# Kernel tuning notes

Measured on AMD Instinct MI355X. Metric: run time of the kernel, lower is better.

The kernel has to match this reference:

```python
import jax, jax.numpy as jnp
import numpy as np

N_PTS = 131072      # query points
N_DIMS = 3          # spatial dims
N_FEATS = 1000      # total_n_features = prod(feature_grid_shape '10,10,10')
FDIM = 64           # n_features per grid point
PE_TERMS = 6        # num_positional_encoding_terms
HID = 128           # nodes_per_layer
OUT = 1             # n_outputs
D_IN = PE_TERMS * N_DIMS * 2 + FDIM  # 100


def _linear_init(k, d_in, d_out):
    # xavier-ish init for a [out, in] torch-style weight
    return jax.random.normal(k, (d_out, d_in), dtype=jnp.float32) * np.float32(1.0 / np.sqrt(d_in))


def setup_inputs() -> dict:
    key = jax.random.key(0)
    ks = jax.random.split(key, 10)
    x = jax.random.uniform(ks[0], (N_PTS, N_DIMS), minval=-1.0, maxval=1.0, dtype=jnp.float32)
    feature_locations = jax.random.uniform(ks[1], (N_FEATS, N_DIMS), minval=-1.0, maxval=1.0, dtype=jnp.float32)
    feature_vectors = jax.random.normal(ks[2], (N_FEATS, FDIM), dtype=jnp.float32)
    W0 = _linear_init(ks[3], D_IN, HID); b0 = jnp.zeros((HID,), jnp.float32)
    W1 = _linear_init(ks[4], HID, HID);  b1 = jnp.zeros((HID,), jnp.float32)
    W2 = _linear_init(ks[5], HID, HID);  b2 = jnp.zeros((HID,), jnp.float32)
    W3 = _linear_init(ks[6], HID, HID);  b3 = jnp.zeros((HID,), jnp.float32)
    W4 = _linear_init(ks[7], HID, OUT);  b4 = jnp.zeros((OUT,), jnp.float32)
    return dict(x=x, feature_locations=feature_locations, feature_vectors=feature_vectors,
                W0=W0, b0=b0, W1=W1, b1=b1, W2=W2, b2=b2, W3=W3, b3=b3, W4=W4, b4=b4)


def _snake_alt(h):
    # SnakeAlt activation: 0.5*x + sin(x)^2
    return 0.5 * h + jnp.sin(h) ** 2


def _positional_encoding(x):
    # NeRF-style PE: sin/cos of (2^l * pi * x), l = 0..PE_TERMS-1 -> [N, PE_TERMS*N_DIMS*2]
    freqs = (2.0 ** jnp.arange(PE_TERMS, dtype=jnp.float32)) * jnp.pi
    ang = x[:, :, None] * freqs  # [N, n_dims, L]
    return jnp.concatenate([jnp.sin(ang), jnp.cos(ang)], axis=-1).reshape(x.shape[0], -1)


def reference(x, feature_locations, feature_vectors, W0, b0, W1, b1, W2, b2, W3, b3, W4, b4):
    # L2 distance from each point to each feature location, via expanded quadratic form
    # (same math as sqrt(sum((x-loc)^2)) without materializing [N, F, n_dims])
    d2 = (jnp.sum(x * x, axis=-1, keepdims=True)
          - 2.0 * (x @ feature_locations.T)
          + jnp.sum(feature_locations * feature_locations, axis=-1))
    d2 = jnp.maximum(d2, 0.0)
    inv_d = 1.0 / (jnp.sqrt(d2) + 1e-6)
    w = jax.nn.softmax(inv_d, axis=1)            # [N, F]
    feats = w @ feature_vectors                  # [N, FDIM]
    pe = _positional_encoding(x)                 # [N, 36]
    y = jnp.concatenate([pe, feats], axis=1)     # [N, 100]
    y = _snake_alt(y @ W0.T + b0)
    y = _snake_alt(y @ W1.T + b1)
    y = _snake_alt(y @ W2.T + b2)
    y = _snake_alt(y @ W3.T + b3)
    return y @ W4.T + b4                         # [N, 1]
```

## Files before the change

### kernel.cpp

```cpp
#include <hip/hip_runtime.h>
#include <hip/hip_bf16.h>

#define N_PTS   131072
#define N_FEATS 1000
#define FDIM    64
#define HID     128
#define NCHUNK  32
#define PI_F    3.14159265358979f
#define L2E     1.44269504f

typedef short  short8  __attribute__((ext_vector_type(8)));
typedef float  floatx4 __attribute__((ext_vector_type(4)));

__device__ __forceinline__ unsigned int packbf2(float a, float b) {
    float2 t; t.x = a; t.y = b;
    __hip_bfloat162 h = __float22bfloat162_rn(t);
    union { __hip_bfloat162 hh; unsigned int u; } cv; cv.hh = h;
    return cv.u;
}
__device__ __forceinline__ unsigned short f2bf(float f) {
    return (unsigned short)packbf2(f, f);
}
__device__ __forceinline__ float bf2f(unsigned short h) {
    return __uint_as_float(((unsigned int)h) << 16);
}
__device__ __forceinline__ floatx4 min3_4(floatx4 a, floatx4 b, floatx4 c) {
    floatx4 r;
    r[0] = fminf(fminf(a[0], b[0]), c[0]);
    r[1] = fminf(fminf(a[1], b[1]), c[1]);
    r[2] = fminf(fminf(a[2], b[2]), c[2]);
    r[3] = fminf(fminf(a[3], b[3]), c[3]);
    return r;
}


__device__ __forceinline__ short8 xfrag_build(int quad, float x0, float x1, float x2) {
    unsigned short h0, m0, l0, h1, m1, l1, h2, m2, l2, Ah, Am, Al;
    { h0 = f2bf(x0); float r = x0 - bf2f(h0); m0 = f2bf(r); l0 = f2bf(r - bf2f(m0)); }
    { h1 = f2bf(x1); float r = x1 - bf2f(h1); m1 = f2bf(r); l1 = f2bf(r - bf2f(m1)); }
    { h2 = f2bf(x2); float r = x2 - bf2f(h2); m2 = f2bf(r); l2 = f2bf(r - bf2f(m2)); }
    float A = x0*x0 + x1*x1 + x2*x2;
    { Ah = f2bf(A); float r = A - bf2f(Ah); Am = f2bf(r); Al = f2bf(r - bf2f(Am)); }
    union { short8 v; unsigned short u[8]; } f;
    if (quad == 0) {
        f.u[0]=h0; f.u[1]=m0; f.u[2]=h0; f.u[3]=l0; f.u[4]=m0; f.u[5]=h0; f.u[6]=h1; f.u[7]=m1;
    } else if (quad == 1) {
        f.u[0]=h1; f.u[1]=l1; f.u[2]=m1; f.u[3]=h1; f.u[4]=h2; f.u[5]=m2; f.u[6]=h2; f.u[7]=l2;
    } else if (quad == 2) {
        f.u[0]=m2; f.u[1]=h2; f.u[2]=0x3F80; f.u[3]=0x3F80; f.u[4]=0x3F80; f.u[5]=Ah; f.u[6]=Am; f.u[7]=Al;
    } else {
        f.v = (short8)0;
    }
    return f.v;
}

__global__ void prep_all(const float* __restrict__ locs, const float* __restrict__ fv,
                         const float* __restrict__ W0, const float* __restrict__ W1,
                         const float* __restrict__ W2, const float* __restrict__ W3,
                         unsigned short* __restrict__ DB,
                         unsigned short* __restrict__ fvB, unsigned short* __restrict__ WB)
{
    int i = blockIdx.x * 256 + threadIdx.x;
    if (i < 65536) {
        int j = i & 7, n = (i >> 3) & 63, cq = i >> 9;
        int c = cq >> 2, quad = cq & 3;
        int fl = (j < 4) ? quad*4 + j : 16 + quad*4 + (j - 4);
        int f = c*32 + fl;
        float v = (f < N_FEATS) ? fv[f*FDIM + n] : 0.f;
        fvB[i] = f2bf(v);
    } else if (i < 131072) {
        int r = i - 65536;
        int j = r & 7, lane = (r >> 3) & 63, c = (r >> 9) & 3;
        int nt = (r >> 11) & 1, q = (r >> 12) & 3, L = r >> 14;
        int n = (q*2 + nt)*16 + (lane & 15);
        int k = c*32 + (lane >> 4)*8 + j;
        const float* W = (L == 0) ? W0 : (L == 1) ? W1 : (L == 2) ? W2 : W3;
        int Kin = (L == 0) ? 100 : 128;
        float v = (k < Kin) ? W[n*Kin + k] : 0.f;
        WB[r] = f2bf(v);
    } else if (i < 163840) {
        int r = i - 131072;
        int j = r & 7, ft = (r >> 3) & 15, quad = (r >> 7) & 3, fg = r >> 9;
        int f = fg*16 + ft, s = quad*8 + j;
        float lx, ly, lz;
        if (f < N_FEATS) { lx = locs[f*3+0]; ly = locs[f*3+1]; lz = locs[f*3+2]; }
        else             { lx = 1e9f; ly = 1e9f; lz = 1e9f; }
        unsigned short val = 0;
        if (s < 18) {
            int d = s / 6, t = s - d*6;
            float l2 = -2.f * ((d == 0) ? lx : (d == 1) ? ly : lz);
            unsigned short h = f2bf(l2);
            float r1 = l2 - bf2f(h);
            unsigned short m = f2bf(r1);
            unsigned short l = f2bf(r1 - bf2f(m));
            val = (t == 2 || t == 4) ? m : (t == 5) ? l : h;
        } else if (s < 21) {
            float SL = lx*lx + ly*ly + lz*lz;
            unsigned short h = f2bf(SL);
            float r1 = SL - bf2f(h);
            unsigned short m = f2bf(r1);
            unsigned short l = f2bf(r1 - bf2f(m));
            val = (s == 18) ? h : (s == 19) ? m : l;
        } else if (s < 24) {
            val = 0x3F80;
        }
        DB[r] = val;
    }
}

__global__ __launch_bounds__(256, 3)
void afvsrn_mfma(const float* __restrict__ x,
                 const unsigned short* __restrict__ DB,
                 const unsigned short* __restrict__ fvB,
                 const unsigned short* __restrict__ WB,
                 const float* __restrict__ b0, const float* __restrict__ b1,
                 const float* __restrict__ b2, const float* __restrict__ b3,
                 const float* __restrict__ W4, const float* __restrict__ b4,
                 float* __restrict__ out)
{
    __shared__ unsigned short act[128 * 136];

    const int lane = threadIdx.x & 63;
    const int wv   = threadIdx.x >> 6;
    const int ptl  = lane & 15;
    const int quad = lane >> 4;
    const int ptbase = blockIdx.x * 128 + wv * 32;

    const float xA0 = x[(ptbase + ptl)*3 + 0];
    const float xA1 = x[(ptbase + ptl)*3 + 1];
    const float xA2 = x[(ptbase + ptl)*3 + 2];
    const float xB0 = x[(ptbase + 16 + ptl)*3 + 0];
    const float xB1 = x[(ptbase + 16 + ptl)*3 + 1];
    const float xB2 = x[(ptbase + 16 + ptl)*3 + 2];

    const short8 xfA = xfrag_build(quad, xA0, xA1, xA2);
    const short8 xfB = xfrag_build(quad, xB0, xB1, xB2);

    const short8* DBp = (const short8*)DB;
    const int dbidx = quad*16 + ptl;
    const floatx4 Z = {0.f, 0.f, 0.f, 0.f};

    floatx4 mnA = {1e30f, 1e30f, 1e30f, 1e30f};
    floatx4 mnB = {1e30f, 1e30f, 1e30f, 1e30f};
    #pragma unroll 2
    for (int c = 0; c < NCHUNK; ++c) {
        short8 a0 = DBp[(2*c    )*64 + dbidx];
        short8 a1 = DBp[(2*c + 1)*64 + dbidx];
        floatx4 dA0 = __builtin_amdgcn_mfma_f32_16x16x32_bf16(a0, xfA, Z, 0, 0, 0);
        floatx4 dA1 = __builtin_amdgcn_mfma_f32_16x16x32_bf16(a1, xfA, Z, 0, 0, 0);
        floatx4 dB0 = __builtin_amdgcn_mfma_f32_16x16x32_bf16(a0, xfB, Z, 0, 0, 0);
        floatx4 dB1 = __builtin_amdgcn_mfma_f32_16x16x32_bf16(a1, xfB, Z, 0, 0, 0);
        mnA = min3_4(mnA, dA0, dA1);
        mnB = min3_4(mnB, dB0, dB1);
    }
    float mdA = fminf(fminf(mnA[0], mnA[1]), fminf(mnA[2], mnA[3]));
    float mdB = fminf(fminf(mnB[0], mnB[1]), fminf(mnB[2], mnB[3]));
    mdA = fminf(mdA, __shfl_xor(mdA, 16));
    mdA = fminf(mdA, __shfl_xor(mdA, 32));
    mdB = fminf(mdB, __shfl_xor(mdB, 16));
    mdB = fminf(mdB, __shfl_xor(mdB, 32));
    const float nmA = -__builtin_amdgcn_rsqf(fmaxf(mdA, 1e-12f)) * L2E;
    const float nmB = -__builtin_amdgcn_rsqf(fmaxf(mdB, 1e-12f)) * L2E;

    const short8 ONES = {0x3F80,0x3F80,0x3F80,0x3F80,0x3F80,0x3F80,0x3F80,0x3F80};
    floatx4 acc2A[4] = {}, acc2B[4] = {};
    floatx4 accLA = {}, accLB = {};
    #pragma unroll 1
    for (int c = 0; c < NCHUNK-1; ++c) {
        const short8* bp = (const short8*)fvB + (c*4 + quad)*64;
        short8 bf0 = bp[ptl];
        short8 bf1 = bp[16 + ptl];
        short8 bf2 = bp[32 + ptl];
        short8 bf3 = bp[48 + ptl];

        short8 a0 = DBp[(2*c    )*64 + dbidx];
        short8 a1 = DBp[(2*c + 1)*64 + dbidx];
        floatx4 dA0 = __builtin_amdgcn_mfma_f32_16x16x32_bf16(a0, xfA, Z, 0, 0, 0);
        floatx4 dA1 = __builtin_amdgcn_mfma_f32_16x16x32_bf16(a1, xfA, Z, 0, 0, 0);
        floatx4 dB0 = __builtin_amdgcn_mfma_f32_16x16x32_bf16(a0, xfB, Z, 0, 0, 0);
        floatx4 dB1 = __builtin_amdgcn_mfma_f32_16x16x32_bf16(a1, xfB, Z, 0, 0, 0);

        union { short8 v; unsigned int u[4]; } afA, afB;
        {
            float p0, p1;
            p0 = __builtin_amdgcn_exp2f(fmaf(__builtin_amdgcn_rsqf(fmaxf(dA0[0], 1e-12f)), L2E, nmA));
            p1 = __builtin_amdgcn_exp2f(fmaf(__builtin_amdgcn_rsqf(fmaxf(dA0[1], 1e-12f)), L2E, nmA));
            afA.u[0] = packbf2(p0, p1);
            p0 = __builtin_amdgcn_exp2f(fmaf(__builtin_amdgcn_rsqf(fmaxf(dA0[2], 1e-12f)), L2E, nmA));
            p1 = __builtin_amdgcn_exp2f(fmaf(__builtin_amdgcn_rsqf(fmaxf(dA0[3], 1e-12f)), L2E, nmA));
            afA.u[1] = packbf2(p0, p1);
            p0 = __builtin_amdgcn_exp2f(fmaf(__builtin_amdgcn_rsqf(fmaxf(dA1[0], 1e-12f)), L2E, nmA));
            p1 = __builtin_amdgcn_exp2f(fmaf(__builtin_amdgcn_rsqf(fmaxf(dA1[1], 1e-12f)), L2E, nmA));
            afA.u[2] = packbf2(p0, p1);
            p0 = __builtin_amdgcn_exp2f(fmaf(__builtin_amdgcn_rsqf(fmaxf(dA1[2], 1e-12f)), L2E, nmA));
            p1 = __builtin_amdgcn_exp2f(fmaf(__builtin_amdgcn_rsqf(fmaxf(dA1[3], 1e-12f)), L2E, nmA));
            afA.u[3] = packbf2(p0, p1);
            p0 = __builtin_amdgcn_exp2f(fmaf(__builtin_amdgcn_rsqf(fmaxf(dB0[0], 1e-12f)), L2E, nmB));
            p1 = __builtin_amdgcn_exp2f(fmaf(__builtin_amdgcn_rsqf(fmaxf(dB0[1], 1e-12f)), L2E, nmB));
            afB.u[0] = packbf2(p0, p1);
            p0 = __builtin_amdgcn_exp2f(fmaf(__builtin_amdgcn_rsqf(fmaxf(dB0[2], 1e-12f)), L2E, nmB));
            p1 = __builtin_amdgcn_exp2f(fmaf(__builtin_amdgcn_rsqf(fmaxf(dB0[3], 1e-12f)), L2E, nmB));
            afB.u[1] = packbf2(p0, p1);
            p0 = __builtin_amdgcn_exp2f(fmaf(__builtin_amdgcn_rsqf(fmaxf(dB1[0], 1e-12f)), L2E, nmB));
            p1 = __builtin_amdgcn_exp2f(fmaf(__builtin_amdgcn_rsqf(fmaxf(dB1[1], 1e-12f)), L2E, nmB));
            afB.u[2] = packbf2(p0, p1);
            p0 = __builtin_amdgcn_exp2f(fmaf(__builtin_amdgcn_rsqf(fmaxf(dB1[2], 1e-12f)), L2E, nmB));
            p1 = __builtin_amdgcn_exp2f(fmaf(__builtin_amdgcn_rsqf(fmaxf(dB1[3], 1e-12f)), L2E, nmB));
            afB.u[3] = packbf2(p0, p1);
        }
        acc2A[0] = __builtin_amdgcn_mfma_f32_16x16x32_bf16(afA.v, bf0, acc2A[0], 0, 0, 0);
        acc2B[0] = __builtin_amdgcn_mfma_f32_16x16x32_bf16(afB.v, bf0, acc2B[0], 0, 0, 0);
        acc2A[1] = __builtin_amdgcn_mfma_f32_16x16x32_bf16(afA.v, bf1, acc2A[1], 0, 0, 0);
        acc2B[1] = __builtin_amdgcn_mfma_f32_16x16x32_bf16(afB.v, bf1, acc2B[1], 0, 0, 0);
        acc2A[2] = __builtin_amdgcn_mfma_f32_16x16x32_bf16(afA.v, bf2, acc2A[2], 0, 0, 0);
        acc2B[2] = __builtin_amdgcn_mfma_f32_16x16x32_bf16(afB.v, bf2, acc2B[2], 0, 0, 0);
        acc2A[3] = __builtin_amdgcn_mfma_f32_16x16x32_bf16(afA.v, bf3, acc2A[3], 0, 0, 0);
        acc2B[3] = __builtin_amdgcn_mfma_f32_16x16x32_bf16(afB.v, bf3, acc2B[3], 0, 0, 0);
        accLA = __builtin_amdgcn_mfma_f32_16x16x32_bf16(afA.v, ONES, accLA, 0, 0, 0);
        accLB = __builtin_amdgcn_mfma_f32_16x16x32_bf16(afB.v, ONES, accLB, 0, 0, 0);
    }
    {
        const int c = NCHUNK-1;
        const short8* bp = (const short8*)fvB + (c*4 + quad)*64;
        short8 bf0 = bp[ptl];
        short8 bf1 = bp[16 + ptl];
        short8 bf2 = bp[32 + ptl];
        short8 bf3 = bp[48 + ptl];

        short8 a0 = DBp[(2*c)*64 + dbidx];
        floatx4 dA0 = __builtin_amdgcn_mfma_f32_16x16x32_bf16(a0, xfA, Z, 0, 0, 0);
        floatx4 dB0 = __builtin_amdgcn_mfma_f32_16x16x32_bf16(a0, xfB, Z, 0, 0, 0);
        const float nmAe = (quad < 2) ? nmA : -__builtin_inff();
        const float nmBe = (quad < 2) ? nmB : -__builtin_inff();
        union { short8 v; unsigned int u[4]; } afA, afB;
        {
            float p0, p1;
            p0 = __builtin_amdgcn_exp2f(fmaf(__builtin_amdgcn_rsqf(fmaxf(dA0[0], 1e-12f)), L2E, nmAe));
            p1 = __builtin_amdgcn_exp2f(fmaf(__builtin_amdgcn_rsqf(fmaxf(dA0[1], 1e-12f)), L2E, nmAe));
            afA.u[0] = packbf2(p0, p1);
            p0 = __builtin_amdgcn_exp2f(fmaf(__builtin_amdgcn_rsqf(fmaxf(dA0[2], 1e-12f)), L2E, nmAe));
            p1 = __builtin_amdgcn_exp2f(fmaf(__builtin_amdgcn_rsqf(fmaxf(dA0[3], 1e-12f)), L2E, nmAe));
            afA.u[1] = packbf2(p0, p1);
            afA.u[2] = 0; afA.u[3] = 0;
            p0 = __builtin_amdgcn_exp2f(fmaf(__builtin_amdgcn_rsqf(fmaxf(dB0[0], 1e-12f)), L2E, nmBe));
            p1 = __builtin_amdgcn_exp2f(fmaf(__builtin_amdgcn_rsqf(fmaxf(dB0[1], 1e-12f)), L2E, nmBe));
            afB.u[0] = packbf2(p0, p1);
            p0 = __builtin_amdgcn_exp2f(fmaf(__builtin_amdgcn_rsqf(fmaxf(dB0[2], 1e-12f)), L2E, nmBe));
            p1 = __builtin_amdgcn_exp2f(fmaf(__builtin_amdgcn_rsqf(fmaxf(dB0[3], 1e-12f)), L2E, nmBe));
            afB.u[1] = packbf2(p0, p1);
            afB.u[2] = 0; afB.u[3] = 0;
        }
        acc2A[0] = __builtin_amdgcn_mfma_f32_16x16x32_bf16(afA.v, bf0, acc2A[0], 0, 0, 0);
        acc2B[0] = __builtin_amdgcn_mfma_f32_16x16x32_bf16(afB.v, bf0, acc2B[0], 0, 0, 0);
        acc2A[1] = __builtin_amdgcn_mfma_f32_16x16x32_bf16(afA.v, bf1, acc2A[1], 0, 0, 0);
        acc2B[1] = __builtin_amdgcn_mfma_f32_16x16x32_bf16(afB.v, bf1, acc2B[1], 0, 0, 0);
        acc2A[2] = __builtin_amdgcn_mfma_f32_16x16x32_bf16(afA.v, bf2, acc2A[2], 0, 0, 0);
        acc2B[2] = __builtin_amdgcn_mfma_f32_16x16x32_bf16(afB.v, bf2, acc2B[2], 0, 0, 0);
        acc2A[3] = __builtin_amdgcn_mfma_f32_16x16x32_bf16(afA.v, bf3, acc2A[3], 0, 0, 0);
        acc2B[3] = __builtin_amdgcn_mfma_f32_16x16x32_bf16(afB.v, bf3, acc2B[3], 0, 0, 0);
        accLA = __builtin_amdgcn_mfma_f32_16x16x32_bf16(afA.v, ONES, accLA, 0, 0, 0);
        accLB = __builtin_amdgcn_mfma_f32_16x16x32_bf16(afB.v, ONES, accLB, 0, 0, 0);
    }

    float linvA[4], linvB[4];
    #pragma unroll
    for (int r = 0; r < 4; ++r) {
        linvA[r] = __builtin_amdgcn_rcpf(accLA[r]);
        linvB[r] = __builtin_amdgcn_rcpf(accLB[r]);
    }

    const int myrowA = (wv*32 + ptl) * 136;
    const int myrowB = (wv*32 + 16 + ptl) * 136;
    *(short8*)&act[myrowA + 96 + quad*8] = (short8)0;
    *(short8*)&act[myrowB + 96 + quad*8] = (short8)0;

    #pragma unroll
    for (int i = 0; i < 9; ++i) {
        int k = quad*9 + i;
        int d = k / 12, r12 = k % 12, l = r12 % 6;
        float fr = PI_F * (float)(1 << l);
        float xvA = (d == 0) ? xA0 : (d == 1) ? xA1 : xA2;
        float xvB = (d == 0) ? xB0 : (d == 1) ? xB1 : xB2;
        float vA = (r12 < 6) ? __sinf(xvA * fr) : __cosf(xvA * fr);
        float vB = (r12 < 6) ? __sinf(xvB * fr) : __cosf(xvB * fr);
        act[myrowA + k] = f2bf(vA);
        act[myrowB + k] = f2bf(vB);
    }

    #pragma unroll
    for (int nt = 0; nt < 4; ++nt)
        #pragma unroll
        for (int r = 0; r < 4; ++r) {
            act[(wv*32 + quad*4 + r)*136 + 36 + nt*16 + ptl]      = f2bf(acc2A[nt][r] * linvA[r]);
            act[(wv*32 + 16 + quad*4 + r)*136 + 36 + nt*16 + ptl] = f2bf(acc2B[nt][r] * linvB[r]);
        }

    short8 aA[4], aB[4];
    #pragma unroll 1
    for (int t = 0; t < 16; ++t) {
        const int L = t >> 2, q = t & 3;
        if (q == 0) {
            #pragma unroll
            for (int c = 0; c < 4; ++c) {
                aA[c] = *(const short8*)&act[myrowA + c*32 + quad*8];
                aB[c] = *(const short8*)&act[myrowB + c*32 + quad*8];
            }
        }
        const float* bL = (L == 0) ? b0 : (L == 1) ? b1 : (L == 2) ? b2 : b3;
        const short8* bp = (const short8*)WB + t*512;
        #pragma unroll
        for (int nt = 0; nt < 2; ++nt) {
            floatx4 accA = {}, accB = {};
            #pragma unroll
            for (int c = 0; c < 4; ++c) {
                short8 bw = bp[(nt*4 + c)*64 + lane];
                accA = __builtin_amdgcn_mfma_f32_16x16x32_bf16(aA[c], bw, accA, 0, 0, 0);
                accB = __builtin_amdgcn_mfma_f32_16x16x32_bf16(aB[c], bw, accB, 0, 0, 0);
            }
            const int col = (q*2 + nt)*16 + ptl;
            const float bias = bL[col];
            #pragma unroll
            for (int r = 0; r < 4; ++r) {
                float hA = accA[r] + bias;
                float hB = accB[r] + bias;
                float sA = __sinf(hA);
                float sB = __sinf(hB);
                hA = 0.5f*hA + sA*sA;
                hB = 0.5f*hB + sB*sB;
                act[(wv*32 + quad*4 + r)*136 + col]      = f2bf(hA);
                act[(wv*32 + 16 + quad*4 + r)*136 + col] = f2bf(hB);
            }
        }
    }

    float oA = 0.f, oB = 0.f;
    #pragma unroll
    for (int s = 0; s < 4; ++s) {
        short8 avA = *(const short8*)&act[myrowA + quad*32 + s*8];
        short8 avB = *(const short8*)&act[myrowB + quad*32 + s*8];
        const floatx4* wp = (const floatx4*)W4 + (quad*32 + s*8)/4;
        floatx4 w0 = wp[0], w1 = wp[1];
        oA = fmaf(bf2f((unsigned short)avA[0]), w0[0], oA);
        oB = fmaf(bf2f((unsigned short)avB[0]), w0[0], oB);
        oA = fmaf(bf2f((unsigned short)avA[1]), w0[1], oA);
        oB = fmaf(bf2f((unsigned short)avB[1]), w0[1], oB);
        oA = fmaf(bf2f((unsigned short)avA[2]), w0[2], oA);
        oB = fmaf(bf2f((unsigned short)avB[2]), w0[2], oB);
        oA = fmaf(bf2f((unsigned short)avA[3]), w0[3], oA);
        oB = fmaf(bf2f((unsigned short)avB[3]), w0[3], oB);
        oA = fmaf(bf2f((unsigned short)avA[4]), w1[0], oA);
        oB = fmaf(bf2f((unsigned short)avB[4]), w1[0], oB);
        oA = fmaf(bf2f((unsigned short)avA[5]), w1[1], oA);
        oB = fmaf(bf2f((unsigned short)avB[5]), w1[1], oB);
        oA = fmaf(bf2f((unsigned short)avA[6]), w1[2], oA);
        oB = fmaf(bf2f((unsigned short)avB[6]), w1[2], oB);
        oA = fmaf(bf2f((unsigned short)avA[7]), w1[3], oA);
        oB = fmaf(bf2f((unsigned short)avB[7]), w1[3], oB);
    }
    oA += __shfl_xor(oA, 16);
    oA += __shfl_xor(oA, 32);
    oB += __shfl_xor(oB, 16);
    oB += __shfl_xor(oB, 32);
    if (quad == 0) {
        float bb = b4[0];
        out[ptbase + ptl]      = oA + bb;
        out[ptbase + 16 + ptl] = oB + bb;
    }
}

extern "C" void kernel_launch(void* const* d_in, const int* in_sizes, int n_in,
                              void* d_out, int out_size, void* d_ws, size_t ws_size,
                              hipStream_t stream)
{
    const float* x  = (const float*)d_in[0];
    const float* lc = (const float*)d_in[1];
    const float* fv = (const float*)d_in[2];
    const float* W0 = (const float*)d_in[3];
    const float* b0 = (const float*)d_in[4];
    const float* W1 = (const float*)d_in[5];
    const float* b1 = (const float*)d_in[6];
    const float* W2 = (const float*)d_in[7];
    const float* b2 = (const float*)d_in[8];
    const float* W3 = (const float*)d_in[9];
    const float* b3 = (const float*)d_in[10];
    const float* W4 = (const float*)d_in[11];
    const float* b4 = (const float*)d_in[12];

    char* ws = (char*)d_ws;
    unsigned short* DBp = (unsigned short*)(ws + 0);
    unsigned short* fvB = (unsigned short*)(ws + 65536);
    unsigned short* WB  = (unsigned short*)(ws + 65536 + 131072);

    prep_all<<<dim3(640), dim3(256), 0, stream>>>(lc, fv, W0, W1, W2, W3,
                                                  DBp, fvB, WB);

    afvsrn_mfma<<<dim3(N_PTS/128), dim3(256), 0, stream>>>(
        x, DBp, fvB, WB, b0, b1, b2, b3, W4, b4, (float*)d_out);
}
```

Before: 157.9 us.

## Process 64 points per wave to reuse B-fragments and fold epsilon into MFMA

Each wave now handles four 16-point tiles instead of two, so every loaded distance-matrix, feature-vector and weight fragment feeds twice as many MFMAs. Blocks cover 256 points, LDS doubles, and launch bounds drop to 2 blocks per CU. A small epsilon is added to the squared distance through an extra bf16 term in the MFMA operands, which removes the per-element fmax clamps before rsq. The trade-off is much higher register pressure and lower occupancy, which could cause spills or less latency hiding.

```diff
diff --git a/kernel.cpp b/kernel.cpp
--- a/kernel.cpp
+++ b/kernel.cpp
@@ -8,6 +8,7 @@
 #define NCHUNK  32
 #define PI_F    3.14159265358979f
 #define L2E     1.44269504f
+#define EPS_D2  4e-7f
 
 typedef short  short8  __attribute__((ext_vector_type(8)));
 typedef float  floatx4 __attribute__((ext_vector_type(4)));
@@ -31,6 +32,11 @@
     r[2] = fminf(fminf(a[2], b[2]), c[2]);
     r[3] = fminf(fminf(a[3], b[3]), c[3]);
     return r;
+}
+__device__ __forceinline__ unsigned int pack_p2(float d0, float d1, float nm) {
+    float p0 = __builtin_amdgcn_exp2f(fmaf(__builtin_amdgcn_rsqf(d0), L2E, nm));
+    float p1 = __builtin_amdgcn_exp2f(fmaf(__builtin_amdgcn_rsqf(d1), L2E, nm));
+    return packbf2(p0, p1);
 }
 
 
@@ -50,6 +56,7 @@
         f.u[0]=m2; f.u[1]=h2; f.u[2]=0x3F80; f.u[3]=0x3F80; f.u[4]=0x3F80; f.u[5]=Ah; f.u[6]=Am; f.u[7]=Al;
     } else {
         f.v = (short8)0;
+        f.u[0] = 0x3F80;
     }
     return f.v;
 }
@@ -103,12 +110,14 @@
             val = (s == 18) ? h : (s == 19) ? m : l;
         } else if (s < 24) {
             val = 0x3F80;
+        } else if (s == 24) {
+            val = f2bf(EPS_D2);
         }
         DB[r] = val;
     }
 }
 
-__global__ __launch_bounds__(256, 3)
+__global__ __launch_bounds__(256, 2)
 void afvsrn_mfma(const float* __restrict__ x,
                  const unsigned short* __restrict__ DB,
                  const unsigned short* __restrict__ fvB,
@@ -118,253 +127,205 @@
                  const float* __restrict__ W4, const float* __restrict__ b4,
                  float* __restrict__ out)
 {
-    __shared__ unsigned short act[128 * 136];
+    __shared__ unsigned short act[256 * 136];
 
     const int lane = threadIdx.x & 63;
     const int wv   = threadIdx.x >> 6;
     const int ptl  = lane & 15;
     const int quad = lane >> 4;
-    const int ptbase = blockIdx.x * 128 + wv * 32;
-
-    const float xA0 = x[(ptbase + ptl)*3 + 0];
-    const float xA1 = x[(ptbase + ptl)*3 + 1];
-    const float xA2 = x[(ptbase + ptl)*3 + 2];
-    const float xB0 = x[(ptbase + 16 + ptl)*3 + 0];
-    const float xB1 = x[(ptbase + 16 + ptl)*3 + 1];
-    const float xB2 = x[(ptbase + 16 + ptl)*3 + 2];
-
-    const short8 xfA = xfrag_build(quad, xA0, xA1, xA2);
-    const short8 xfB = xfrag_build(quad, xB0, xB1, xB2);
+    const int ptbase = blockIdx.x * 256 + wv * 64;
+
+    float x0[4], x1[4], x2[4];
+    #pragma unroll
+    for (int t = 0; t < 4; ++t) {
+        x0[t] = x[(ptbase + t*16 + ptl)*3 + 0];
+        x1[t] = x[(ptbase + t*16 + ptl)*3 + 1];
+        x2[t] = x[(ptbase + t*16 + ptl)*3 + 2];
+    }
+    short8 xf[4];
+    #pragma unroll
+    for (int t = 0; t < 4; ++t) xf[t] = xfrag_build(quad, x0[t], x1[t], x2[t]);
 
     const short8* DBp = (const short8*)DB;
     const int dbidx = quad*16 + ptl;
     const floatx4 Z = {0.f, 0.f, 0.f, 0.f};
 
-    floatx4 mnA = {1e30f, 1e30f, 1e30f, 1e30f};
-    floatx4 mnB = {1e30f, 1e30f, 1e30f, 1e30f};
+    floatx4 mn[4];
+    #pragma unroll
+    for (int t = 0; t < 4; ++t) { mn[t][0]=1e30f; mn[t][1]=1e30f; mn[t][2]=1e30f; mn[t][3]=1e30f; }
     #pragma unroll 2
     for (int c = 0; c < NCHUNK; ++c) {
         short8 a0 = DBp[(2*c    )*64 + dbidx];
         short8 a1 = DBp[(2*c + 1)*64 + dbidx];
-        floatx4 dA0 = __builtin_amdgcn_mfma_f32_16x16x32_bf16(a0, xfA, Z, 0, 0, 0);
-        floatx4 dA1 = __builtin_amdgcn_mfma_f32_16x16x32_bf16(a1, xfA, Z, 0, 0, 0);
-        floatx4 dB0 = __builtin_amdgcn_mfma_f32_16x16x32_bf16(a0, xfB, Z, 0, 0, 0);
-        floatx4 dB1 = __builtin_amdgcn_mfma_f32_16x16x32_bf16(a1, xfB, Z, 0, 0, 0);
-        mnA = min3_4(mnA, dA0, dA1);
-        mnB = min3_4(mnB, dB0, dB1);
-    }
-    float mdA = fminf(fminf(mnA[0], mnA[1]), fminf(mnA[2], mnA[3]));
-    float mdB = fminf(fminf(mnB[0], mnB[1]), fminf(mnB[2], mnB[3]));
-    mdA = fminf(mdA, __shfl_xor(mdA, 16));
-    mdA = fminf(mdA, __shfl_xor(mdA, 32));
-    mdB = fminf(mdB, __shfl_xor(mdB, 16));
-    mdB = fminf(mdB, __shfl_xor(mdB, 32));
-    const float nmA = -__builtin_amdgcn_rsqf(fmaxf(mdA, 1e-12f)) * L2E;
-    const float nmB = -__builtin_amdgcn_rsqf(fmaxf(mdB, 1e-12f)) * L2E;
+        #pragma unroll
+        for (int t = 0; t < 4; ++t) {
+            floatx4 d0 = __builtin_amdgcn_mfma_f32_16x16x32_bf16(a0, xf[t], Z, 0, 0, 0);
+            floatx4 d1 = __builtin_amdgcn_mfma_f32_16x16x32_bf16(a1, xf[t], Z, 0, 0, 0);
+            mn[t] = min3_4(mn[t], d0, d1);
+        }
+    }
+    float nm[4];
+    #pragma unroll
+    for (int t = 0; t < 4; ++t) {
+        float md = fminf(fminf(mn[t][0], mn[t][1]), fminf(mn[t][2], mn[t][3]));
+        md = fminf(md, __shfl_xor(md, 16));
+        md = fminf(md, __shfl_xor(md, 32));
+        nm[t] = -__builtin_amdgcn_rsqf(md) * L2E;
+    }
 
     const short8 ONES = {0x3F80,0x3F80,0x3F80,0x3F80,0x3F80,0x3F80,0x3F80,0x3F80};
-    floatx4 acc2A[4] = {}, acc2B[4] = {};
-    floatx4 accLA = {}, accLB = {};
+    floatx4 acc2[4][4] = {};
+    floatx4 accL[4] = {};
     #pragma unroll 1
     for (int c = 0; c < NCHUNK-1; ++c) {
         const short8* bp = (const short8*)fvB + (c*4 + quad)*64;
-        short8 bf0 = bp[ptl];
-        short8 bf1 = bp[16 + ptl];
-        short8 bf2 = bp[32 + ptl];
-        short8 bf3 = bp[48 + ptl];
-
+        short8 bfv0 = bp[ptl];
+        short8 bfv1 = bp[16 + ptl];
+        short8 bfv2 = bp[32 + ptl];
+        short8 bfv3 = bp[48 + ptl];
         short8 a0 = DBp[(2*c    )*64 + dbidx];
         short8 a1 = DBp[(2*c + 1)*64 + dbidx];
-        floatx4 dA0 = __builtin_amdgcn_mfma_f32_16x16x32_bf16(a0, xfA, Z, 0, 0, 0);
-        floatx4 dA1 = __builtin_amdgcn_mfma_f32_16x16x32_bf16(a1, xfA, Z, 0, 0, 0);
-        floatx4 dB0 = __builtin_amdgcn_mfma_f32_16x16x32_bf16(a0, xfB, Z, 0, 0, 0);
-        floatx4 dB1 = __builtin_amdgcn_mfma_f32_16x16x32_bf16(a1, xfB, Z, 0, 0, 0);
-
-        union { short8 v; unsigned int u[4]; } afA, afB;
-        {
-            float p0, p1;
-            p0 = __builtin_amdgcn_exp2f(fmaf(__builtin_amdgcn_rsqf(fmaxf(dA0[0], 1e-12f)), L2E, nmA));
-            p1 = __builtin_amdgcn_exp2f(fmaf(__builtin_amdgcn_rsqf(fmaxf(dA0[1], 1e-12f)), L2E, nmA));
-            afA.u[0] = packbf2(p0, p1);
-            p0 = __builtin_amdgcn_exp2f(fmaf(__builtin_amdgcn_rsqf(fmaxf(dA0[2], 1e-12f)), L2E, nmA));
-            p1 = __builtin_amdgcn_exp2f(fmaf(__builtin_amdgcn_rsqf(fmaxf(dA0[3], 1e-12f)), L2E, nmA));
-            afA.u[1] = packbf2(p0, p1);
-            p0 = __builtin_amdgcn_exp2f(fmaf(__builtin_amdgcn_rsqf(fmaxf(dA1[0], 1e-12f)), L2E, nmA));
-            p1 = __builtin_amdgcn_exp2f(fmaf(__builtin_amdgcn_rsqf(fmaxf(dA1[1], 1e-12f)), L2E, nmA));
-            afA.u[2] = packbf2(p0, p1);
-            p0 = __builtin_amdgcn_exp2f(fmaf(__builtin_amdgcn_rsqf(fmaxf(dA1[2], 1e-12f)), L2E, nmA));
-            p1 = __builtin_amdgcn_exp2f(fmaf(__builtin_amdgcn_rsqf(fmaxf(dA1[3], 1e-12f)), L2E, nmA));
-            afA.u[3] = packbf2(p0, p1);
-            p0 = __builtin_amdgcn_exp2f(fmaf(__builtin_amdgcn_rsqf(fmaxf(dB0[0], 1e-12f)), L2E, nmB));
-            p1 = __builtin_amdgcn_exp2f(fmaf(__builtin_amdgcn_rsqf(fmaxf(dB0[1], 1e-12f)), L2E, nmB));
-            afB.u[0] = packbf2(p0, p1);
-            p0 = __builtin_amdgcn_exp2f(fmaf(__builtin_amdgcn_rsqf(fmaxf(dB0[2], 1e-12f)), L2E, nmB));
-            p1 = __builtin_amdgcn_exp2f(fmaf(__builtin_amdgcn_rsqf(fmaxf(dB0[3], 1e-12f)), L2E, nmB));
-            afB.u[1] = packbf2(p0, p1);
-            p0 = __builtin_amdgcn_exp2f(fmaf(__builtin_amdgcn_rsqf(fmaxf(dB1[0], 1e-12f)), L2E, nmB));
-            p1 = __builtin_amdgcn_exp2f(fmaf(__builtin_amdgcn_rsqf(fmaxf(dB1[1], 1e-12f)), L2E, nmB));
-            afB.u[2] = packbf2(p0, p1);
-            p0 = __builtin_amdgcn_exp2f(fmaf(__builtin_amdgcn_rsqf(fmaxf(dB1[2], 1e-12f)), L2E, nmB));
-            p1 = __builtin_amdgcn_exp2f(fmaf(__builtin_amdgcn_rsqf(fmaxf(dB1[3], 1e-12f)), L2E, nmB));
-            afB.u[3] = packbf2(p0, p1);
-        }
-        acc2A[0] = __builtin_amdgcn_mfma_f32_16x16x32_bf16(afA.v, bf0, acc2A[0], 0, 0, 0);
-        acc2B[0] = __builtin_amdgcn_mfma_f32_16x16x32_bf16(afB.v, bf0, acc2B[0], 0, 0, 0);
-        acc2A[1] = __builtin_amdgcn_mfma_f32_16x16x32_bf16(afA.v, bf1, acc2A[1], 0, 0, 0);
-        acc2B[1] = __builtin_amdgcn_mfma_f32_16x16x32_bf16(afB.v, bf1, acc2B[1], 0, 0, 0);
-        acc2A[2] = __builtin_amdgcn_mfma_f32_16x16x32_bf16(afA.v, bf2, acc2A[2], 0, 0, 0);
-        acc2B[2] = __builtin_amdgcn_mfma_f32_16x16x32_bf16(afB.v, bf2, acc2B[2], 0, 0, 0);
-        acc2A[3] = __builtin_amdgcn_mfma_f32_16x16x32_bf16(afA.v, bf3, acc2A[3], 0, 0, 0);
-        acc2B[3] = __builtin_amdgcn_mfma_f32_16x16x32_bf16(afB.v, bf3, acc2B[3], 0, 0, 0);
-        accLA = __builtin_amdgcn_mfma_f32_16x16x32_bf16(afA.v, ONES, accLA, 0, 0, 0);
-        accLB = __builtin_amdgcn_mfma_f32_16x16x32_bf16(afB.v, ONES, accLB, 0, 0, 0);
+        #pragma unroll
+        for (int t = 0; t < 4; ++t) {
+            floatx4 d0 = __builtin_amdgcn_mfma_f32_16x16x32_bf16(a0, xf[t], Z, 0, 0, 0);
+            floatx4 d1 = __builtin_amdgcn_mfma_f32_16x16x32_bf16(a1, xf[t], Z, 0, 0, 0);
+            union { short8 v; unsigned int u[4]; } af;
+            af.u[0] = pack_p2(d0[0], d0[1], nm[t]);
+            af.u[1] = pack_p2(d0[2], d0[3], nm[t]);
+            af.u[2] = pack_p2(d1[0], d1[1], nm[t]);
+            af.u[3] = pack_p2(d1[2], d1[3], nm[t]);
+            acc2[t][0] = __builtin_amdgcn_mfma_f32_16x16x32_bf16(af.v, bfv0, acc2[t][0], 0, 0, 0);
+            acc2[t][1] = __builtin_amdgcn_mfma_f32_16x16x32_bf16(af.v, bfv1, acc2[t][1], 0, 0, 0);
+            acc2[t][2] = __builtin_amdgcn_mfma_f32_16x16x32_bf16(af.v, bfv2, acc2[t][2], 0, 0, 0);
+            acc2[t][3] = __builtin_amdgcn_mfma_f32_16x16x32_bf16(af.v, bfv3, acc2[t][3], 0, 0, 0);
+            accL[t]    = __builtin_amdgcn_mfma_f32_16x16x32_bf16(af.v, ONES, accL[t], 0, 0, 0);
+        }
     }
     {
         const int c = NCHUNK-1;
         const short8* bp = (const short8*)fvB + (c*4 + quad)*64;
-        short8 bf0 = bp[ptl];
-        short8 bf1 = bp[16 + ptl];
-        short8 bf2 = bp[32 + ptl];
-        short8 bf3 = bp[48 + ptl];
-
+        short8 bfv0 = bp[ptl];
+        short8 bfv1 = bp[16 + ptl];
+        short8 bfv2 = bp[32 + ptl];
+        short8 bfv3 = bp[48 + ptl];
         short8 a0 = DBp[(2*c)*64 + dbidx];
-        floatx4 dA0 = __builtin_amdgcn_mfma_f32_16x16x32_bf16(a0, xfA, Z, 0, 0, 0);
-        floatx4 dB0 = __builtin_amdgcn_mfma_f32_16x16x32_bf16(a0, xfB, Z, 0, 0, 0);
-        const float nmAe = (quad < 2) ? nmA : -__builtin_inff();
-        const float nmBe = (quad < 2) ? nmB : -__builtin_inff();
-        union { short8 v; unsigned int u[4]; } afA, afB;
-        {
-            float p0, p1;
-            p0 = __builtin_amdgcn_exp2f(fmaf(__builtin_amdgcn_rsqf(fmaxf(dA0[0], 1e-12f)), L2E, nmAe));
-            p1 = __builtin_amdgcn_exp2f(fmaf(__builtin_amdgcn_rsqf(fmaxf(dA0[1], 1e-12f)), L2E, nmAe));
-            afA.u[0] = packbf2(p0, p1);
-            p0 = __builtin_amdgcn_exp2f(fmaf(__builtin_amdgcn_rsqf(fmaxf(dA0[2], 1e-12f)), L2E, nmAe));
-            p1 = __builtin_amdgcn_exp2f(fmaf(__builtin_amdgcn_rsqf(fmaxf(dA0[3], 1e-12f)), L2E, nmAe));
-            afA.u[1] = packbf2(p0, p1);
-            afA.u[2] = 0; afA.u[3] = 0;
-            p0 = __builtin_amdgcn_exp2f(fmaf(__builtin_amdgcn_rsqf(fmaxf(dB0[0], 1e-12f)), L2E, nmBe));
-            p1 = __builtin_amdgcn_exp2f(fmaf(__builtin_amdgcn_rsqf(fmaxf(dB0[1], 1e-12f)), L2E, nmBe));
-            afB.u[0] = packbf2(p0, p1);
-            p0 = __builtin_amdgcn_exp2f(fmaf(__builtin_amdgcn_rsqf(fmaxf(dB0[2], 1e-12f)), L2E, nmBe));
-            p1 = __builtin_amdgcn_exp2f(fmaf(__builtin_amdgcn_rsqf(fmaxf(dB0[3], 1e-12f)), L2E, nmBe));
-            afB.u[1] = packbf2(p0, p1);
-            afB.u[2] = 0; afB.u[3] = 0;
-        }
-        acc2A[0] = __builtin_amdgcn_mfma_f32_16x16x32_bf16(afA.v, bf0, acc2A[0], 0, 0, 0);
-        acc2B[0] = __builtin_amdgcn_mfma_f32_16x16x32_bf16(afB.v, bf0, acc2B[0], 0, 0, 0);
-        acc2A[1] = __builtin_amdgcn_mfma_f32_16x16x32_bf16(afA.v, bf1, acc2A[1], 0, 0, 0);
-        acc2B[1] = __builtin_amdgcn_mfma_f32_16x16x32_bf16(afB.v, bf1, acc2B[1], 0, 0, 0);
-        acc2A[2] = __builtin_amdgcn_mfma_f32_16x16x32_bf16(afA.v, bf2, acc2A[2], 0, 0, 0);
-        acc2B[2] = __builtin_amdgcn_mfma_f32_16x16x32_bf16(afB.v, bf2, acc2B[2], 0, 0, 0);
-        acc2A[3] = __builtin_amdgcn_mfma_f32_16x16x32_bf16(afA.v, bf3, acc2A[3], 0, 0, 0);
-        acc2B[3] = __builtin_amdgcn_mfma_f32_16x16x32_bf16(afB.v, bf3, acc2B[3], 0, 0, 0);
-        accLA = __builtin_amdgcn_mfma_f32_16x16x32_bf16(afA.v, ONES, accLA, 0, 0, 0);
-        accLB = __builtin_amdgcn_mfma_f32_16x16x32_bf16(afB.v, ONES, accLB, 0, 0, 0);
-    }
-
-    float linvA[4], linvB[4];
-    #pragma unroll
-    for (int r = 0; r < 4; ++r) {
-        linvA[r] = __builtin_amdgcn_rcpf(accLA[r]);
-        linvB[r] = __builtin_amdgcn_rcpf(accLB[r]);
-    }
-
-    const int myrowA = (wv*32 + ptl) * 136;
-    const int myrowB = (wv*32 + 16 + ptl) * 136;
-    *(short8*)&act[myrowA + 96 + quad*8] = (short8)0;
-    *(short8*)&act[myrowB + 96 + quad*8] = (short8)0;
+        #pragma unroll
+        for (int t = 0; t < 4; ++t) {
+            floatx4 d0 = __builtin_amdgcn_mfma_f32_16x16x32_bf16(a0, xf[t], Z, 0, 0, 0);
+            const float nme = (quad < 2) ? nm[t] : -__builtin_inff();
+            union { short8 v; unsigned int u[4]; } af;
+            af.u[0] = pack_p2(d0[0], d0[1], nme);
+            af.u[1] = pack_p2(d0[2], d0[3], nme);
+            af.u[2] = 0; af.u[3] = 0;
+            acc2[t][0] = __builtin_amdgcn_mfma_f32_16x16x32_bf16(af.v, bfv0, acc2[t][0], 0, 0, 0);
+            acc2[t][1] = __builtin_amdgcn_mfma_f32_16x16x32_bf16(af.v, bfv1, acc2[t][1], 0, 0, 0);
+            acc2[t][2] = __builtin_amdgcn_mfma_f32_16x16x32_bf16(af.v, bfv2, acc2[t][2], 0, 0, 0);
+            acc2[t][3] = __builtin_amdgcn_mfma_f32_16x16x32_bf16(af.v, bfv3, acc2[t][3], 0, 0, 0);
+            accL[t]    = __builtin_amdgcn_mfma_f32_16x16x32_bf16(af.v, ONES, accL[t], 0, 0, 0);
+        }
+    }
+
+    float linv[4][4];
+    #pragma unroll
+    for (int t = 0; t < 4; ++t)
+        #pragma unroll
+        for (int r = 0; r < 4; ++r)
+            linv[t][r] = __builtin_amdgcn_rcpf(accL[t][r]);
+
+    int myrow[4];
+    #pragma unroll
+    for (int t = 0; t < 4; ++t) {
+        myrow[t] = (wv*64 + t*16 + ptl) * 136;
+        *(short8*)&act[myrow[t] + 96 + quad*8] = (short8)0;
+    }
 
     #pragma unroll
     for (int i = 0; i < 9; ++i) {
         int k = quad*9 + i;
         int d = k / 12, r12 = k % 12, l = r12 % 6;
         float fr = PI_F * (float)(1 << l);
-        float xvA = (d == 0) ? xA0 : (d == 1) ? xA1 : xA2;
-        float xvB = (d == 0) ? xB0 : (d == 1) ? xB1 : xB2;
-        float vA = (r12 < 6) ? __sinf(xvA * fr) : __cosf(xvA * fr);
-        float vB = (r12 < 6) ? __sinf(xvB * fr) : __cosf(xvB * fr);
-        act[myrowA + k] = f2bf(vA);
-        act[myrowB + k] = f2bf(vB);
+        #pragma unroll
+        for (int t = 0; t < 4; ++t) {
+            float xv = (d == 0) ? x0[t] : (d == 1) ? x1[t] : x2[t];
+            float v = (r12 < 6) ? __sinf(xv * fr) : __cosf(xv * fr);
+            act[myrow[t] + k] = f2bf(v);
+        }
     }
 
     #pragma unroll
     for (int nt = 0; nt < 4; ++nt)
         #pragma unroll
-        for (int r = 0; r < 4; ++r) {
-            act[(wv*32 + quad*4 + r)*136 + 36 + nt*16 + ptl]      = f2bf(acc2A[nt][r] * linvA[r]);
-            act[(wv*32 + 16 + quad*4 + r)*136 + 36 + nt*16 + ptl] = f2bf(acc2B[nt][r] * linvB[r]);
-        }
-
-    short8 aA[4], aB[4];
+        for (int r = 0; r < 4; ++r)
+            #pragma unroll
+            for (int t = 0; t < 4; ++t)
+                act[(wv*64 + t*16 + quad*4 + r)*136 + 36 + nt*16 + ptl] =
+                    f2bf(acc2[t][nt][r] * linv[t][r]);
+
+    short8 a[4][4];
     #pragma unroll 1
-    for (int t = 0; t < 16; ++t) {
-        const int L = t >> 2, q = t & 3;
+    for (int st = 0; st < 16; ++st) {
+        const int L = st >> 2, q = st & 3;
         if (q == 0) {
             #pragma unroll
-            for (int c = 0; c < 4; ++c) {
-                aA[c] = *(const short8*)&act[myrowA + c*32 + quad*8];
-                aB[c] = *(const short8*)&act[myrowB + c*32 + quad*8];
-            }
+            for (int t = 0; t < 4; ++t)
+                #pragma unroll
+                for (int c = 0; c < 4; ++c)
+                    a[t][c] = *(const short8*)&act[myrow[t] + c*32 + quad*8];
         }
         const float* bL = (L == 0) ? b0 : (L == 1) ? b1 : (L == 2) ? b2 : b3;
-        const short8* bp = (const short8*)WB + t*512;
+        const short8* bp = (const short8*)WB + st*512;
         #pragma unroll
         for (int nt = 0; nt < 2; ++nt) {
-            floatx4 accA = {}, accB = {};
+            floatx4 ac[4] = {};
             #pragma unroll
             for (int c = 0; c < 4; ++c) {
                 short8 bw = bp[(nt*4 + c)*64 + lane];
-                accA = __builtin_amdgcn_mfma_f32_16x16x32_bf16(aA[c], bw, accA, 0, 0, 0);
-                accB = __builtin_amdgcn_mfma_f32_16x16x32_bf16(aB[c], bw, accB, 0, 0, 0);
+                #pragma unroll
+                for (int t = 0; t < 4; ++t)
+                    ac[t] = __builtin_amdgcn_mfma_f32_16x16x32_bf16(a[t][c], bw, ac[t], 0, 0, 0);
             }
             const int col = (q*2 + nt)*16 + ptl;
             const float bias = bL[col];
             #pragma unroll
-            for (int r = 0; r < 4; ++r) {
-                float hA = accA[r] + bias;
-                float hB = accB[r] + bias;
-                float sA = __sinf(hA);
-                float sB = __sinf(hB);
-                hA = 0.5f*hA + sA*sA;
-                hB = 0.5f*hB + sB*sB;
-                act[(wv*32 + quad*4 + r)*136 + col]      = f2bf(hA);
-                act[(wv*32 + 16 + quad*4 + r)*136 + col] = f2bf(hB);
-            }
-        }
-    }
-
-    float oA = 0.f, oB = 0.f;
-    #pragma unroll
-    for (int s = 0; s < 4; ++s) {
-        short8 avA = *(const short8*)&act[myrowA + quad*32 + s*8];
-        short8 avB = *(const short8*)&act[myrowB + quad*32 + s*8];
-        const floatx4* wp = (const floatx4*)W4 + (quad*32 + s*8)/4;
+            for (int t = 0; t < 4; ++t)
+                #pragma unroll
+                for (int r = 0; r < 4; ++r) {
+                    float h = ac[t][r] + bias;
+                    float s = __sinf(h);
+                    h = 0.5f*h + s*s;
+                    act[(wv*64 + t*16 + quad*4 + r)*136 + col] = f2bf(h);
+                }
+        }
+    }
+
+    float o[4] = {0.f, 0.f, 0.f, 0.f};
+    #pragma unroll
+    for (int sg = 0; sg < 4; ++sg) {
+        const floatx4* wp = (const floatx4*)W4 + (quad*32 + sg*8)/4;
         floatx4 w0 = wp[0], w1 = wp[1];
-        oA = fmaf(bf2f((unsigned short)avA[0]), w0[0], oA);
-        oB = fmaf(bf2f((unsigned short)avB[0]), w0[0], oB);
-        oA = fmaf(bf2f((unsigned short)avA[1]), w0[1], oA);
-        oB = fmaf(bf2f((unsigned short)avB[1]), w0[1], oB);
-        oA = fmaf(bf2f((unsigned short)avA[2]), w0[2], oA);
-        oB = fmaf(bf2f((unsigned short)avB[2]), w0[2], oB);
-        oA = fmaf(bf2f((unsigned short)avA[3]), w0[3], oA);
-        oB = fmaf(bf2f((unsigned short)avB[3]), w0[3], oB);
-        oA = fmaf(bf2f((unsigned short)avA[4]), w1[0], oA);
-        oB = fmaf(bf2f((unsigned short)avB[4]), w1[0], oB);
-        oA = fmaf(bf2f((unsigned short)avA[5]), w1[1], oA);
-        oB = fmaf(bf2f((unsigned short)avB[5]), w1[1], oB);
-        oA = fmaf(bf2f((unsigned short)avA[6]), w1[2], oA);
-        oB = fmaf(bf2f((unsigned short)avB[6]), w1[2], oB);
-        oA = fmaf(bf2f((unsigned short)avA[7]), w1[3], oA);
-        oB = fmaf(bf2f((unsigned short)avB[7]), w1[3], oB);
-    }
-    oA += __shfl_xor(oA, 16);
-    oA += __shfl_xor(oA, 32);
-    oB += __shfl_xor(oB, 16);
-    oB += __shfl_xor(oB, 32);
+        #pragma unroll
+        for (int t = 0; t < 4; ++t) {
+            short8 av = *(const short8*)&act[myrow[t] + quad*32 + sg*8];
+            o[t] = fmaf(bf2f((unsigned short)av[0]), w0[0], o[t]);
+            o[t] = fmaf(bf2f((unsigned short)av[1]), w0[1], o[t]);
+            o[t] = fmaf(bf2f((unsigned short)av[2]), w0[2], o[t]);
+            o[t] = fmaf(bf2f((unsigned short)av[3]), w0[3], o[t]);
+            o[t] = fmaf(bf2f((unsigned short)av[4]), w1[0], o[t]);
+            o[t] = fmaf(bf2f((unsigned short)av[5]), w1[1], o[t]);
+            o[t] = fmaf(bf2f((unsigned short)av[6]), w1[2], o[t]);
+            o[t] = fmaf(bf2f((unsigned short)av[7]), w1[3], o[t]);
+        }
+    }
+    #pragma unroll
+    for (int t = 0; t < 4; ++t) {
+        o[t] += __shfl_xor(o[t], 16);
+        o[t] += __shfl_xor(o[t], 32);
+    }
     if (quad == 0) {
         float bb = b4[0];
-        out[ptbase + ptl]      = oA + bb;
-        out[ptbase + 16 + ptl] = oB + bb;
+        #pragma unroll
+        for (int t = 0; t < 4; ++t)
+            out[ptbase + t*16 + ptl] = o[t] + bb;
     }
 }
 
@@ -394,6 +355,6 @@
     prep_all<<<dim3(640), dim3(256), 0, stream>>>(lc, fv, W0, W1, W2, W3,
                                                   DBp, fvB, WB);
 
-    afvsrn_mfma<<<dim3(N_PTS/128), dim3(256), 0, stream>>>(
+    afvsrn_mfma<<<dim3(N_PTS/256), dim3(256), 0, stream>>>(
         x, DBp, fvB, WB, b0, b1, b2, b3, W4, b4, (float*)d_out);
 }
```

Result: faster. 149.2 us (-5.5%).
